# Kernel optimization log

Hardware: AMD Instinct MI355X
Metric: run time of the kernel (lower is better)

Reference implementation:

```python
import jax, jax.numpy as jnp
import numpy as np

B, N, DX, E, H, HD, KH, FF = 8, 8192, 2, 128, 8, 16, 32, 128
G1, G2, PMAX = 32, 32, 32


def _ln(x, g, b):
    mu = jnp.mean(x, axis=-1, keepdims=True)
    var = jnp.mean((x - mu) ** 2, axis=-1, keepdims=True)
    return (x - mu) * jax.lax.rsqrt(var + 1e-5) * g + b


def _cumcount_row(idx):
    # for each element, number of earlier elements with the same value (stable)
    n = idx.shape[0]
    order = jnp.argsort(idx)  # stable
    si = idx[order]
    ar = jnp.arange(n)
    is_start = jnp.concatenate([jnp.ones((1,), bool), si[1:] != si[:-1]])
    seg_start = jax.lax.associative_scan(jnp.maximum, jnp.where(is_start, ar, 0))
    return jnp.zeros(n, jnp.int32).at[order].set((ar - seg_start).astype(jnp.int32))


def _forward(x, z, latent, Wq, Wk, Wv, Wo, bo, kW1, kb1, kW2, kb2,
             lnq_g, lnq_b, lnk_g, lnk_b, ln2_g, ln2_b, fW1, fb1, fW2, fb2,
             grid_n1, grid_n2, max_patch, num_heads):
    Bb, Nn, dx = x.shape
    e = latent.shape[0]
    dims = (grid_n1, grid_n2)
    M = grid_n1 * grid_n2
    P = max_patch
    h = num_heads
    hd = Wq.shape[1] // h
    # grid range from data (margin = 0), regular grid via linspace
    mins = [jnp.min(x[:, :, i]) for i in range(dx)]
    maxs = [jnp.max(x[:, :, i]) for i in range(dx)]
    axes = [jnp.linspace(mins[i], maxs[i], dims[i]) for i in range(dx)]
    x_grid = jnp.stack(jnp.meshgrid(*axes, indexing="ij"), axis=-1)  # [G1,G2,dx]
    x_grid_flat = x_grid.reshape(M, dx)
    # nearest grid cell per point: regular grid -> per-dim rounding
    flat = None
    for i in range(dx):
        step = (maxs[i] - mins[i]) / (dims[i] - 1)
        ii = jnp.clip(jnp.round((x[..., i] - mins[i]) / step), 0, dims[i] - 1).astype(jnp.int32)
        flat = ii if flat is None else flat * dims[i] + ii
    cell = flat  # [B,N]
    cumc = jax.vmap(_cumcount_row)(cell)          # slot within cell
    slot = jnp.where(cumc < P, cumc, P)           # overflow -> dummy slot (dropped)
    bidx = jnp.broadcast_to(jnp.arange(Bb)[:, None], (Bb, Nn))
    # scatter points into per-cell padded neighbour sets [B, M, P, d]
    jx = jnp.zeros((Bb, M, P + 1, dx), x.dtype).at[bidx, cell, slot].set(x)[:, :, :P]
    jz = jnp.zeros((Bb, M, P + 1, e), z.dtype).at[bidx, cell, slot].set(z)[:, :, :P]
    msk = jnp.zeros((Bb, M, P + 1), bool).at[bidx, cell, slot].set(True)[:, :, :P]
    xg = jnp.broadcast_to(x_grid_flat[None], (Bb, M, dx))
    zg = jnp.broadcast_to(latent[None, None, :], (Bb, M, e))
    # concatenate_x_grid=True: grid token prepended, always attended
    joint_x = jnp.concatenate([xg[:, :, None, :], jx], axis=2).reshape(Bb * M, P + 1, dx)
    joint_z = jnp.concatenate([zg[:, :, None, :], jz], axis=2).reshape(Bb * M, P + 1, e)
    att_mask = jnp.concatenate([jnp.ones((Bb, M, 1), bool), msk], axis=2).reshape(Bb * M, P + 1)
    xq = xg.reshape(Bb * M, 1, dx)
    zq = zg.reshape(Bb * M, 1, e)
    T = Bb * M
    # masked translation-equivariant cross-attention (pre-norm layer)
    q = jnp.einsum("tqe,ef->tqf", _ln(zq, lnq_g, lnq_b), Wq).reshape(T, 1, h, hd)
    zk_n = _ln(joint_z, lnk_g, lnk_b)
    k = jnp.einsum("tke,ef->tkf", zk_n, Wk).reshape(T, P + 1, h, hd)
    v = jnp.einsum("tke,ef->tkf", zk_n, Wv).reshape(T, P + 1, h, hd)
    dots = jnp.einsum("tqhd,tkhd->thqk", q, k) / jnp.sqrt(jnp.asarray(hd, q.dtype))
    diff = joint_x[:, None, :, :] - xq[:, :, None, :]            # [T,1,P+1,dx]
    kb = jnp.maximum(diff @ kW1 + kb1, 0.0) @ kW2 + kb2          # kernel bias [T,1,P+1,h]
    dots = dots + jnp.transpose(kb, (0, 3, 1, 2))
    dots = jnp.where(att_mask[:, None, None, :], dots, -1e9)
    A = jax.nn.softmax(dots, axis=-1)                            # [T,h,1,P+1]
    out = jnp.einsum("thqk,tkhd->tqhd", A, v).reshape(T, 1, h * hd)
    z_new = zq + out @ Wo + bo
    z_new = z_new + (jnp.maximum(_ln(z_new, ln2_g, ln2_b) @ fW1 + fb1, 0.0) @ fW2 + fb2)
    x_new = jnp.einsum("tqk,tkd->tqd", jnp.mean(A, axis=1), joint_x)  # TE location update
    x_grid_out = x_new.reshape(Bb, grid_n1, grid_n2, dx)
    z_grid_out = z_new.reshape(Bb, grid_n1, grid_n2, e)
    return (x_grid_out, z_grid_out)


def setup_inputs():
    key = jax.random.key(0)
    ks = jax.random.split(key, 12)
    s = 0.05
    return {
        "x": jax.random.uniform(ks[0], (B, N, DX), jnp.float32),
        "z": jax.random.normal(ks[1], (B, N, E), jnp.float32),
        "grid_n1": G1, "grid_n2": G2, "max_patch": PMAX, "num_heads": H,
        "latent": jax.random.normal(ks[2], (E,), jnp.float32),
        "Wq": jax.random.normal(ks[3], (E, H * HD), jnp.float32) * s,
        "Wk": jax.random.normal(ks[4], (E, H * HD), jnp.float32) * s,
        "Wv": jax.random.normal(ks[5], (E, H * HD), jnp.float32) * s,
        "Wo": jax.random.normal(ks[6], (H * HD, E), jnp.float32) * s,
        "bo": jnp.zeros((E,), jnp.float32),
        "kW1": jax.random.normal(ks[7], (DX, KH), jnp.float32) * s,
        "kb1": jnp.zeros((KH,), jnp.float32),
        "kW2": jax.random.normal(ks[8], (KH, H), jnp.float32) * s,
        "kb2": jnp.zeros((H,), jnp.float32),
        "lnq_g": jnp.ones((E,), jnp.float32), "lnq_b": jnp.zeros((E,), jnp.float32),
        "lnk_g": jnp.ones((E,), jnp.float32), "lnk_b": jnp.zeros((E,), jnp.float32),
        "ln2_g": jnp.ones((E,), jnp.float32), "ln2_b": jnp.zeros((E,), jnp.float32),
        "fW1": jax.random.normal(ks[9], (E, FF), jnp.float32) * s,
        "fb1": jnp.zeros((FF,), jnp.float32),
        "fW2": jax.random.normal(ks[10], (FF, E), jnp.float32) * s,
        "fb2": jnp.zeros((E,), jnp.float32),
    }


def reference(x, z, grid_n1, grid_n2, max_patch, num_heads, latent, Wq, Wk, Wv, Wo, bo,
              kW1, kb1, kW2, kb2, lnq_g, lnq_b, lnk_g, lnk_b, ln2_g, ln2_b,
              fW1, fb1, fW2, fb2):
    return _forward(x, z, latent, Wq, Wk, Wv, Wo, bo, kW1, kb1, kW2, kb2,
                    lnq_g, lnq_b, lnk_g, lnk_b, ln2_g, ln2_b, fW1, fb1, fW2, fb2,
                    grid_n1, grid_n2, max_patch, num_heads)
```

## Files before the change

### kernel.cpp

```cpp
#include <hip/hip_runtime.h>
#include <stdint.h>

#define NB 8
#define NN 8192
#define NE 128
#define NH 8
#define NHD 16
#define NKH 32
#define NFF 128
#define NG 32
#define NM 1024
#define NP 32
#define NT 8192
#define NPTS 65536

typedef __attribute__((ext_vector_type(8))) short bf16x8_t;
typedef __attribute__((ext_vector_type(4))) float f32x4_t;

#define WS_MM      0
#define WS_D0      64
#define WS_Q       128
#define WS_VG      640
#define WS_PART    1152
#define WS_CNT     2048
#define WS_CELL    34816
#define WS_PIDX    296960
#define WS_WVT     1345536
#define WS_WOT     1411072
#define WS_FW1T    1443840
#define WS_FW2T    1476608
#define WS_WKQT    1509376
#define WS_SCORES  1513472
#define WS_KV      4194304

__device__ __forceinline__ unsigned short f2bf(float f) {
    unsigned u = __float_as_uint(f);
    u += 0x7FFFu + ((u >> 16) & 1u);
    return (unsigned short)(u >> 16);
}
__device__ __forceinline__ float bflo(unsigned w) { return __uint_as_float(w << 16); }
__device__ __forceinline__ float bfhi(unsigned w) { return __uint_as_float(w & 0xFFFF0000u); }

__global__ __launch_bounds__(256) void k_setup(
        const float* __restrict__ x,
        const float* __restrict__ Wk, const float* __restrict__ Wv, const float* __restrict__ Wo,
        const float* __restrict__ fW1, const float* __restrict__ fW2,
        const float* __restrict__ latent, const float* __restrict__ Wq,
        const float* __restrict__ lnq_g, const float* __restrict__ lnq_b,
        const float* __restrict__ lnk_g, const float* __restrict__ lnk_b,
        const float* __restrict__ kb1, const float* __restrict__ kW2, const float* __restrict__ kb2,
        int* __restrict__ cnt,
        unsigned short* __restrict__ WvT, unsigned short* __restrict__ WoT,
        unsigned short* __restrict__ fW1T, unsigned short* __restrict__ fW2T,
        float* __restrict__ ws_q, float* __restrict__ ws_vg, float* __restrict__ ws_d0,
        unsigned short* __restrict__ WkqT,
        float4* __restrict__ part) {
    int blk = blockIdx.x;
    int t = threadIdx.x;
    if (blk < 16) {
        __shared__ float s_t[64][65];
        const float* src; unsigned short* dst;
        int n0, k0;
        if (blk < 4) {
            int tn = blk >> 1, tk = blk & 1;
            n0 = tn * 64; k0 = tk * 64;
            src = Wv; dst = WvT;
        } else {
            int m = (blk - 4) >> 2, s4 = (blk - 4) & 3;
            int tn = s4 >> 1, tk = s4 & 1;
            n0 = tn * 64; k0 = tk * 64;
            src = (m == 0) ? Wo : (m == 1) ? fW1 : fW2;
            dst = (m == 0) ? WoT : (m == 1) ? fW1T : fW2T;
        }
        int tx = t & 63, ty = t >> 6;
        #pragma unroll
        for (int r = 0; r < 16; ++r) {
            int kr = r * 4 + ty;
            s_t[kr][tx] = src[(k0 + kr) * 128 + n0 + tx];
        }
        __syncthreads();
        #pragma unroll
        for (int r = 0; r < 16; ++r) {
            int nr = r * 4 + ty;
            dst[(n0 + nr) * 128 + k0 + tx] = f2bf(s_t[tx][nr]);
        }
    } else if (blk < 48) {
        int idx = (blk - 16) * 256 + t;
        cnt[idx] = 0;
    } else if (blk == 48) {
        __shared__ float s_qn[128], s_kn[128], s_q[128], s_kg[128];
        __shared__ float s_mu, s_rstd;
        if (t < 64) {
            float v0 = latent[t], v1 = latent[t + 64];
            float s = v0 + v1;
            for (int m = 32; m > 0; m >>= 1) s += __shfl_xor(s, m);
            float mu = s * (1.0f / 128.0f);
            float d0 = v0 - mu, d1 = v1 - mu;
            float q = d0 * d0 + d1 * d1;
            for (int m = 32; m > 0; m >>= 1) q += __shfl_xor(q, m);
            if (t == 0) { s_mu = mu; s_rstd = rsqrtf(q * (1.0f / 128.0f) + 1e-5f); }
        }
        __syncthreads();
        if (t < 128) {
            float nv = (latent[t] - s_mu) * s_rstd;
            s_qn[t] = nv * lnq_g[t] + lnq_b[t];
            s_kn[t] = nv * lnk_g[t] + lnk_b[t];
        }
        __syncthreads();
        if (t < 128) {
            float aq = 0.f, ak = 0.f, av = 0.f;
            for (int e = 0; e < 128; ++e) {
                aq += s_qn[e] * Wq[e * 128 + t];
                ak += s_kn[e] * Wk[e * 128 + t];
                av += s_kn[e] * Wv[e * 128 + t];
            }
            s_q[t] = aq; s_kg[t] = ak;
            ws_q[t] = aq; ws_vg[t] = av;
        }
        __syncthreads();
        if (t < 128) {
            const float* wr = Wk + t * 128;
            #pragma unroll
            for (int h = 0; h < 8; ++h) {
                float a = 0.f;
                #pragma unroll
                for (int d = 0; d < 16; ++d) a += wr[h * 16 + d] * s_q[h * 16 + d];
                WkqT[h * 128 + t] = f2bf(a * 0.25f);
                WkqT[(h + 8) * 128 + t] = 0;
            }
        }
        if (t < 8) {
            float acc = 0.f;
            for (int d = 0; d < 16; ++d) acc += s_q[t * 16 + d] * s_kg[t * 16 + d];
            float kb0 = kb2[t];
            for (int j = 0; j < 32; ++j) kb0 += fmaxf(kb1[j], 0.f) * kW2[j * 8 + t];
            ws_d0[t] = acc * 0.25f + kb0;
        }
    } else {
        __shared__ float s_red[4][4];
        int pb = blk - 49;
        const float4* xp = (const float4*)x + pb * 1024;
        float mn0 = 1e30f, mx0 = -1e30f, mn1 = 1e30f, mx1 = -1e30f;
        #pragma unroll
        for (int it = 0; it < 4; ++it) {
            float4 v = xp[it * 256 + t];
            mn0 = fminf(mn0, fminf(v.x, v.z)); mx0 = fmaxf(mx0, fmaxf(v.x, v.z));
            mn1 = fminf(mn1, fminf(v.y, v.w)); mx1 = fmaxf(mx1, fmaxf(v.y, v.w));
        }
        #pragma unroll
        for (int m = 32; m > 0; m >>= 1) {
            mn0 = fminf(mn0, __shfl_xor(mn0, m)); mx0 = fmaxf(mx0, __shfl_xor(mx0, m));
            mn1 = fminf(mn1, __shfl_xor(mn1, m)); mx1 = fmaxf(mx1, __shfl_xor(mx1, m));
        }
        int w = t >> 6;
        if ((t & 63) == 0) {
            s_red[w][0] = mn0; s_red[w][1] = mn1; s_red[w][2] = mx0; s_red[w][3] = mx1;
        }
        __syncthreads();
        if (t == 0) {
            float a0 = fminf(fminf(s_red[0][0], s_red[1][0]), fminf(s_red[2][0], s_red[3][0]));
            float a1 = fminf(fminf(s_red[0][1], s_red[1][1]), fminf(s_red[2][1], s_red[3][1]));
            float b0 = fmaxf(fmaxf(s_red[0][2], s_red[1][2]), fmaxf(s_red[2][2], s_red[3][2]));
            float b1 = fmaxf(fmaxf(s_red[0][3], s_red[1][3]), fmaxf(s_red[2][3], s_red[3][3]));
            part[pb] = make_float4(a0, a1, b0, b1);
        }
    }
}

__global__ __launch_bounds__(256) void k_binkv(
        const float* __restrict__ x, const float* __restrict__ z,
        const float4* __restrict__ part, float* __restrict__ mm,
        const float* __restrict__ lnk_g, const float* __restrict__ lnk_b,
        const unsigned short* __restrict__ WkqT,
        const float* __restrict__ kW1, const float* __restrict__ kb1,
        const float* __restrict__ kW2, const float* __restrict__ kb2,
        const unsigned short* __restrict__ WvT, unsigned short* __restrict__ kv,
        float* __restrict__ scores,
        int* __restrict__ cell, int* __restrict__ cnt, int* __restrict__ ptIdx) {
    int t = threadIdx.x;
    if (blockIdx.x >= 1024) {
        int l = t & 63;
        float mn0 = 1e30f, mn1 = 1e30f, mx0 = -1e30f, mx1 = -1e30f;
        if (l < 32) { float4 p = part[l]; mn0 = p.x; mn1 = p.y; mx0 = p.z; mx1 = p.w; }
        #pragma unroll
        for (int m = 32; m > 0; m >>= 1) {
            mn0 = fminf(mn0, __shfl_xor(mn0, m)); mx0 = fmaxf(mx0, __shfl_xor(mx0, m));
            mn1 = fminf(mn1, __shfl_xor(mn1, m)); mx1 = fmaxf(mx1, __shfl_xor(mx1, m));
        }
        if (blockIdx.x == 1024 && t == 0) {
            mm[0] = mn0; mm[1] = mn1; mm[2] = mx0; mm[3] = mx1;
        }
        int i = (blockIdx.x - 1024) * 256 + t;
        float st0 = (mx0 - mn0) / 31.0f, st1 = (mx1 - mn1) / 31.0f;
        float2 xv = ((const float2*)x)[i];
        int i0 = (int)rintf((xv.x - mn0) / st0); i0 = min(max(i0, 0), 31);
        int i1 = (int)rintf((xv.y - mn1) / st1); i1 = min(max(i1, 0), 31);
        int c = i0 * 32 + i1;
        cell[i] = c;
        int bb = i >> 13;
        int slot = atomicAdd(&cnt[bb * NM + c], 1);
        if (slot < NP) ptIdx[(bb * NM + c) * NP + slot] = i & (NN - 1);
        return;
    }
    __shared__ unsigned short s_zn[64][136];
    __shared__ unsigned short s_stage[4][16][68];
    int w = t >> 6, lane = t & 63;
    long base = (long)blockIdx.x * 64;
    int sub = lane >> 5;
    int lq = lane & 31;
    int mrow = lane & 15, quad = lane >> 4;

    float mn0 = 1e30f, mn1 = 1e30f, mx0 = -1e30f, mx1 = -1e30f;
    if (lane < 32) { float4 p = part[lane]; mn0 = p.x; mn1 = p.y; mx0 = p.z; mx1 = p.w; }
    #pragma unroll
    for (int m = 32; m > 0; m >>= 1) {
        mn0 = fminf(mn0, __shfl_xor(mn0, m)); mx0 = fmaxf(mx0, __shfl_xor(mx0, m));
        mn1 = fminf(mn1, __shfl_xor(mn1, m)); mx1 = fmaxf(mx1, __shfl_xor(mx1, m));
    }
    int ptl = w * 16 + mrow;
    float2 xv2 = ((const float2*)x)[base + ptl];

    int th = w >> 1, fh = w & 1;
    bf16x8_t afrag[4][4];
    #pragma unroll
    for (int j = 0; j < 4; ++j) {
        const unsigned short* ap = WvT + ((fh * 4 + j) * 16 + mrow) * 128 + quad * 8;
        #pragma unroll
        for (int kc = 0; kc < 4; ++kc)
            afrag[j][kc] = *(const bf16x8_t*)(ap + kc * 32);
    }
    bf16x8_t sfrag[4];
    #pragma unroll
    for (int kc = 0; kc < 4; ++kc)
        sfrag[kc] = *(const bf16x8_t*)(WkqT + mrow * 128 + kc * 32 + quad * 8);

    float4 g4 = ((const float4*)lnk_g)[lq];
    float4 b4 = ((const float4*)lnk_b)[lq];
    float4 v[8];
    #pragma unroll
    for (int i = 0; i < 8; ++i) {
        int pl = w * 16 + i * 2 + sub;
        v[i] = ((const float4*)z)[(base + pl) * 32 + lq];
    }
    #pragma unroll
    for (int i = 0; i < 8; ++i) {
        int pl = w * 16 + i * 2 + sub;
        float sum = v[i].x + v[i].y + v[i].z + v[i].w;
        float ssq = v[i].x * v[i].x + v[i].y * v[i].y + v[i].z * v[i].z + v[i].w * v[i].w;
        #pragma unroll
        for (int m = 1; m < 32; m <<= 1) {
            sum += __shfl_xor(sum, m);
            ssq += __shfl_xor(ssq, m);
        }
        float mu = sum * (1.0f / 128.0f);
        float var = fmaxf(ssq * (1.0f / 128.0f) - mu * mu, 0.0f);
        float rstd = rsqrtf(var + 1e-5f);
        float n0 = (v[i].x - mu) * rstd * g4.x + b4.x;
        float n1 = (v[i].y - mu) * rstd * g4.y + b4.y;
        float n2 = (v[i].z - mu) * rstd * g4.z + b4.z;
        float n3 = (v[i].w - mu) * rstd * g4.w + b4.w;
        unsigned d0 = (unsigned)f2bf(n0) | ((unsigned)f2bf(n1) << 16);
        unsigned d1 = (unsigned)f2bf(n2) | ((unsigned)f2bf(n3) << 16);
        *(uint2*)&s_zn[pl][lq * 4] = make_uint2(d0, d1);
    }
    __syncthreads();

    #pragma unroll
    for (int tau = 0; tau < 2; ++tau) {
        int trow = th * 32 + tau * 16;
        bf16x8_t bfrag[4];
        #pragma unroll
        for (int kc = 0; kc < 4; ++kc)
            bfrag[kc] = *(const bf16x8_t*)&s_zn[trow + mrow][kc * 32 + quad * 8];
        #pragma unroll
        for (int j = 0; j < 4; ++j) {
            f32x4_t acc = {0.f, 0.f, 0.f, 0.f};
            #pragma unroll
            for (int kc = 0; kc < 4; ++kc)
                acc = __builtin_amdgcn_mfma_f32_16x16x32_bf16(afrag[j][kc], bfrag[kc], acc, 0, 0, 0);
            unsigned d0 = (unsigned)f2bf(acc[0]) | ((unsigned)f2bf(acc[1]) << 16);
            unsigned d1 = (unsigned)f2bf(acc[2]) | ((unsigned)f2bf(acc[3]) << 16);
            *(uint2*)&s_stage[w][mrow][j * 16 + quad * 4] = make_uint2(d0, d1);
        }
        int tok = lane >> 3, u = lane & 7;
        long tk0 = base + trow;
        uint4 ra = *(const uint4*)&s_stage[w][tok][u * 8];
        *(uint4*)(kv + (tk0 + tok) * 128 + fh * 64 + u * 8) = ra;
        uint4 rb = *(const uint4*)&s_stage[w][tok + 8][u * 8];
        *(uint4*)(kv + (tk0 + tok + 8) * 128 + fh * 64 + u * 8) = rb;
    }

    f32x4_t sacc = {0.f, 0.f, 0.f, 0.f};
    {
        bf16x8_t sb[4];
        #pragma unroll
        for (int kc = 0; kc < 4; ++kc)
            sb[kc] = *(const bf16x8_t*)&s_zn[w * 16 + mrow][kc * 32 + quad * 8];
        #pragma unroll
        for (int kc = 0; kc < 4; ++kc)
            sacc = __builtin_amdgcn_mfma_f32_16x16x32_bf16(sfrag[kc], sb[kc], sacc, 0, 0, 0);
    }

    {
        float st0 = (mx0 - mn0) / 31.0f, st1 = (mx1 - mn1) / 31.0f;
        int i0 = (int)rintf((xv2.x - mn0) / st0); i0 = min(max(i0, 0), 31);
        int i1 = (int)rintf((xv2.y - mn1) / st1); i1 = min(max(i1, 0), 31);
        float cx0 = (i0 == 31) ? mx0 : mn0 + i0 * st0;
        float cx1 = (i1 == 31) ? mx1 : mn1 + i1 * st1;
        float d0 = xv2.x - cx0, d1 = xv2.y - cx1;
        float k0 = 0.f, k1 = 0.f, k2 = 0.f, k3 = 0.f, k4 = 0.f, k5 = 0.f, k6 = 0.f, k7 = 0.f;
        #pragma unroll
        for (int jj = 0; jj < 8; ++jj) {
            int j = quad * 8 + jj;
            float hj = fmaf(d0, kW1[j], fmaf(d1, kW1[32 + j], kb1[j]));
            hj = fmaxf(hj, 0.f);
            float4 w2a = *(const float4*)(kW2 + j * 8);
            float4 w2b = *(const float4*)(kW2 + j * 8 + 4);
            k0 = fmaf(hj, w2a.x, k0); k1 = fmaf(hj, w2a.y, k1);
            k2 = fmaf(hj, w2a.z, k2); k3 = fmaf(hj, w2a.w, k3);
            k4 = fmaf(hj, w2b.x, k4); k5 = fmaf(hj, w2b.y, k5);
            k6 = fmaf(hj, w2b.z, k6); k7 = fmaf(hj, w2b.w, k7);
        }
        k0 += __shfl_xor(k0, 16); k0 += __shfl_xor(k0, 32);
        k1 += __shfl_xor(k1, 16); k1 += __shfl_xor(k1, 32);
        k2 += __shfl_xor(k2, 16); k2 += __shfl_xor(k2, 32);
        k3 += __shfl_xor(k3, 16); k3 += __shfl_xor(k3, 32);
        k4 += __shfl_xor(k4, 16); k4 += __shfl_xor(k4, 32);
        k5 += __shfl_xor(k5, 16); k5 += __shfl_xor(k5, 32);
        k6 += __shfl_xor(k6, 16); k6 += __shfl_xor(k6, 32);
        k7 += __shfl_xor(k7, 16); k7 += __shfl_xor(k7, 32);
        if (quad == 0) {
            float4 kb2v = ((const float4*)kb2)[0];
            float4 o;
            o.x = sacc[0] + k0 + kb2v.x; o.y = sacc[1] + k1 + kb2v.y;
            o.z = sacc[2] + k2 + kb2v.z; o.w = sacc[3] + k3 + kb2v.w;
            *(float4*)(scores + ((size_t)(base + ptl)) * 8) = o;
        } else if (quad == 1) {
            float4 kb2v = ((const float4*)kb2)[1];
            float4 o;
            o.x = sacc[0] + k4 + kb2v.x; o.y = sacc[1] + k5 + kb2v.y;
            o.z = sacc[2] + k6 + kb2v.z; o.w = sacc[3] + k7 + kb2v.w;
            *(float4*)(scores + ((size_t)(base + ptl)) * 8 + 4) = o;
        }
    }
}

__global__ __launch_bounds__(256) void k_attn(const float* __restrict__ x,
        const int* __restrict__ cell, const int* __restrict__ cnt, int* __restrict__ ptIdx,
        const float* __restrict__ mm, const unsigned short* __restrict__ kv,
        const float* __restrict__ scores,
        const float* __restrict__ ws_vg, const float* __restrict__ ws_d0,
        const float* __restrict__ latent, const float* __restrict__ bo,
        const float* __restrict__ ln2_g, const float* __restrict__ ln2_b,
        const float* __restrict__ fb1, const float* __restrict__ fb2,
        const unsigned short* __restrict__ WoT, const unsigned short* __restrict__ fW1T,
        const unsigned short* __restrict__ fW2T,
        float* __restrict__ xout, float* __restrict__ zout) {
    __shared__ unsigned short s_a[16][136];
    __shared__ unsigned short s_a2[16][136];
    __shared__ float s_z[4][128];
    __shared__ float s_lat[128], s_g2[128], s_b2[128], s_fb1v[128], s_fb2v[128];
    int t = threadIdx.x;
    int l = t & 63;
    int w = t >> 6;
    if (t < 128) {
        s_lat[t] = latent[t] + bo[t];
        s_g2[t] = ln2_g[t]; s_b2[t] = ln2_b[t];
        s_fb1v[t] = fb1[t]; s_fb2v[t] = fb2[t];
    }
    int bm = blockIdx.x * 4 + w;
    int b = bm >> 10;
    int h = l >> 3, jp = l & 7;

    float mn0 = mm[0], mn1 = mm[1], mx0 = mm[2], mx1 = mm[3];
    int i0 = (bm & 1023) >> 5, i1 = bm & 31;
    float st0 = (mx0 - mn0) / 31.0f, st1 = (mx1 - mn1) / 31.0f;
    float xg0 = (i0 == 31) ? mx0 : mn0 + i0 * st0;
    float xg1 = (i1 == 31) ? mx1 : mn1 + i1 * st1;
    int craw = cnt[bm];
    int c = min(craw, NP);
    if (craw > NP) {
        int mycell = bm & 1023;
        const int* cb = cell + b * NN;
        int run = 0;
        for (int ch = 0; ch < NN / 64 && run < NP; ++ch) {
            int n = ch * 64 + l;
            bool match = (cb[n] == mycell);
            unsigned long long mask = __ballot(match);
            if (match) {
                int rank = run + __popcll(mask & ((1ull << l) - 1ull));
                if (rank < NP) ptIdx[bm * NP + rank] = n;
            }
            run += __popcll(mask);
        }
    }

    float vg0 = ws_vg[2 * l], vg1 = ws_vg[2 * l + 1];
    float ag = ws_d0[h];

    int idxreg = 0; float x0r = 0.f, x1r = 0.f;
    if (l < c) {
        idxreg = ptIdx[bm * NP + l];
        float2 xv = ((const float2*)x)[(size_t)b * NN + idxreg];
        x0r = xv.x; x1r = xv.y;
    }

    float areg[4];
    areg[0] = areg[1] = areg[2] = areg[3] = -1e30f;
    #pragma unroll
    for (int g = 0; g < 4; ++g) {
        if (c > g * 8) {
            int key = g * 8 + jp;
            int idxk = __shfl(idxreg, key);
            if (key < c)
                areg[g] = scores[((size_t)b * NN + idxk) * 8 + h];
        }
    }
    unsigned vreg[16];
    #pragma unroll
    for (int g = 0; g < 2; ++g) {
        if (c > g * 8) {
            #pragma unroll
            for (int k8 = 0; k8 < 8; ++k8) {
                int key = g * 8 + k8;
                if (key < c) {
                    int idxk = __shfl(idxreg, key);
                    vreg[key] = ((const unsigned*)kv)[((size_t)(b * NN + idxk) << 6) + l];
                }
            }
        }
    }

    float mx = fmaxf(fmaxf(areg[0], areg[1]), fmaxf(areg[2], areg[3]));
    mx = fmaxf(mx, ag);
    mx = fmaxf(mx, __shfl_xor(mx, 1));
    mx = fmaxf(mx, __shfl_xor(mx, 2));
    mx = fmaxf(mx, __shfl_xor(mx, 4));
    float e0 = __expf(areg[0] - mx), e1 = __expf(areg[1] - mx);
    float e2 = __expf(areg[2] - mx), e3 = __expf(areg[3] - mx);
    float eg = __expf(ag - mx);
    float s = e0 + e1 + e2 + e3;
    s += __shfl_xor(s, 1);
    s += __shfl_xor(s, 2);
    s += __shfl_xor(s, 4);
    s += eg;
    float inv = 1.0f / s;

    float accA = eg * inv * vg0, accB = eg * inv * vg1;
    #pragma unroll
    for (int g = 0; g < 2; ++g) {
        if (c > g * 8) {
            float em = (g == 0) ? e0 : e1;
            #pragma unroll
            for (int k8 = 0; k8 < 8; ++k8) {
                int key = g * 8 + k8;
                if (key < c) {
                    float a = __shfl(em, (l & 56) | k8) * inv;
                    unsigned vw = vreg[key];
                    accA = fmaf(a, bflo(vw), accA);
                    accB = fmaf(a, bfhi(vw), accB);
                }
            }
        }
    }
    #pragma unroll
    for (int g = 2; g < 4; ++g) {
        if (c > g * 8) {
            float em = (g == 2) ? e2 : e3;
            #pragma unroll
            for (int k8 = 0; k8 < 8; ++k8) {
                int key = g * 8 + k8;
                if (key < c) {
                    int idxk = __shfl(idxreg, key);
                    const unsigned* rowp = (const unsigned*)kv + ((size_t)(b * NN + idxk) << 6);
                    unsigned vw = rowp[l];
                    float a = __shfl(em, (l & 56) | k8) * inv;
                    accA = fmaf(a, bflo(vw), accA);
                    accB = fmaf(a, bfhi(vw), accB);
                }
            }
        }
    }
    unsigned ow = ((unsigned)f2bf(accB) << 16) | (unsigned)f2bf(accA);
    *(unsigned*)&s_a[w][2 * l] = ow;

    float s0 = e0 * inv, s1 = e1 * inv, s2 = e2 * inv, s3 = e3 * inv, sg = eg * inv;
    #pragma unroll
    for (int m = 8; m <= 32; m <<= 1) {
        s0 += __shfl_xor(s0, m); s1 += __shfl_xor(s1, m);
        s2 += __shfl_xor(s2, m); s3 += __shfl_xor(s3, m);
        sg += __shfl_xor(sg, m);
    }
    float px0 = 0.f, px1 = 0.f;
    {
        float xx0, xx1;
        xx0 = __shfl(x0r, jp);      xx1 = __shfl(x1r, jp);
        px0 = fmaf(s0, xx0, px0);   px1 = fmaf(s0, xx1, px1);
        xx0 = __shfl(x0r, jp + 8);  xx1 = __shfl(x1r, jp + 8);
        px0 = fmaf(s1, xx0, px0);   px1 = fmaf(s1, xx1, px1);
        xx0 = __shfl(x0r, jp + 16); xx1 = __shfl(x1r, jp + 16);
        px0 = fmaf(s2, xx0, px0);   px1 = fmaf(s2, xx1, px1);
        xx0 = __shfl(x0r, jp + 24); xx1 = __shfl(x1r, jp + 24);
        px0 = fmaf(s3, xx0, px0);   px1 = fmaf(s3, xx1, px1);
    }
    px0 += __shfl_xor(px0, 1); px1 += __shfl_xor(px1, 1);
    px0 += __shfl_xor(px0, 2); px1 += __shfl_xor(px1, 2);
    px0 += __shfl_xor(px0, 4); px1 += __shfl_xor(px1, 4);
    if (l == 0) {
        xout[bm * 2]     = (px0 + sg * xg0) * 0.125f;
        xout[bm * 2 + 1] = (px1 + sg * xg1) * 0.125f;
    }

    __syncthreads();
    int mrow = l & 15, quad = l >> 4;
    int base4 = blockIdx.x * 4;
    {
        bf16x8_t a[4];
        #pragma unroll
        for (int kc = 0; kc < 4; ++kc)
            a[kc] = *(const bf16x8_t*)&s_a[mrow][kc * 32 + quad * 8];
        #pragma unroll
        for (int cc = 0; cc < 2; ++cc) {
            int ct = w * 2 + cc;
            f32x4_t acc = {0.f, 0.f, 0.f, 0.f};
            const unsigned short* bp = WoT + (ct * 16 + mrow) * 128 + quad * 8;
            #pragma unroll
            for (int kc = 0; kc < 4; ++kc)
                acc = __builtin_amdgcn_mfma_f32_16x16x32_bf16(a[kc], *(const bf16x8_t*)(bp + kc * 32), acc, 0, 0, 0);
            if (quad == 0) {
                int f = ct * 16 + mrow;
                #pragma unroll
                for (int r = 0; r < 4; ++r) s_z[r][f] = acc[r] + s_lat[f];
            }
        }
    }
    __syncthreads();
    {
        float v0 = s_z[w][l], v1 = s_z[w][l + 64];
        float ssum = v0 + v1;
        #pragma unroll
        for (int m = 32; m > 0; m >>= 1) ssum += __shfl_xor(ssum, m);
        float mu = ssum * (1.0f / 128.0f);
        float d0 = v0 - mu, d1 = v1 - mu;
        float qq = d0 * d0 + d1 * d1;
        #pragma unroll
        for (int m = 32; m > 0; m >>= 1) qq += __shfl_xor(qq, m);
        float rstd = rsqrtf(qq * (1.0f / 128.0f) + 1e-5f);
        s_a2[w][l]      = f2bf(d0 * rstd * s_g2[l] + s_b2[l]);
        s_a2[w][l + 64] = f2bf(d1 * rstd * s_g2[l + 64] + s_b2[l + 64]);
    }
    __syncthreads();
    {
        bf16x8_t a[4];
        #pragma unroll
        for (int kc = 0; kc < 4; ++kc)
            a[kc] = *(const bf16x8_t*)&s_a2[mrow][kc * 32 + quad * 8];
        #pragma unroll
        for (int cc = 0; cc < 2; ++cc) {
            int ct = w * 2 + cc;
            f32x4_t acc = {0.f, 0.f, 0.f, 0.f};
            const unsigned short* bp = fW1T + (ct * 16 + mrow) * 128 + quad * 8;
            #pragma unroll
            for (int kc = 0; kc < 4; ++kc)
                acc = __builtin_amdgcn_mfma_f32_16x16x32_bf16(a[kc], *(const bf16x8_t*)(bp + kc * 32), acc, 0, 0, 0);
            if (quad == 0) {
                int f = ct * 16 + mrow;
                #pragma unroll
                for (int r = 0; r < 4; ++r)
                    s_a[r][f] = f2bf(fmaxf(acc[r] + s_fb1v[f], 0.f));
            }
        }
    }
    __syncthreads();
    {
        bf16x8_t a[4];
        #pragma unroll
        for (int kc = 0; kc < 4; ++kc)
            a[kc] = *(const bf16x8_t*)&s_a[mrow][kc * 32 + quad * 8];
        #pragma unroll
        for (int cc = 0; cc < 2; ++cc) {
            int ct = w * 2 + cc;
            f32x4_t acc = {0.f, 0.f, 0.f, 0.f};
            const unsigned short* bp = fW2T + (ct * 16 + mrow) * 128 + quad * 8;
            #pragma unroll
            for (int kc = 0; kc < 4; ++kc)
                acc = __builtin_amdgcn_mfma_f32_16x16x32_bf16(a[kc], *(const bf16x8_t*)(bp + kc * 32), acc, 0, 0, 0);
            if (quad == 0) {
                int f = ct * 16 + mrow;
                #pragma unroll
                for (int r = 0; r < 4; ++r)
                    zout[(base4 + r) * 128 + f] = s_z[r][f] + acc[r] + s_fb2v[f];
            }
        }
    }
}

extern "C" void kernel_launch(void* const* d_in, const int* in_sizes, int n_in,
                              void* d_out, int out_size, void* d_ws, size_t ws_size,
                              hipStream_t stream) {
    const float* x     = (const float*)d_in[0];
    const float* z     = (const float*)d_in[1];
    const float* latent= (const float*)d_in[6];
    const float* Wq    = (const float*)d_in[7];
    const float* Wk    = (const float*)d_in[8];
    const float* Wv    = (const float*)d_in[9];
    const float* Wo    = (const float*)d_in[10];
    const float* bo    = (const float*)d_in[11];
    const float* kW1   = (const float*)d_in[12];
    const float* kb1   = (const float*)d_in[13];
    const float* kW2   = (const float*)d_in[14];
    const float* kb2   = (const float*)d_in[15];
    const float* lnq_g = (const float*)d_in[16];
    const float* lnq_b = (const float*)d_in[17];
    const float* lnk_g = (const float*)d_in[18];
    const float* lnk_b = (const float*)d_in[19];
    const float* ln2_g = (const float*)d_in[20];
    const float* ln2_b = (const float*)d_in[21];
    const float* fW1   = (const float*)d_in[22];
    const float* fb1   = (const float*)d_in[23];
    const float* fW2   = (const float*)d_in[24];
    const float* fb2   = (const float*)d_in[25];

    uint8_t* ws = (uint8_t*)d_ws;
    float* mm     = (float*)(ws + WS_MM);
    float* ws_d0  = (float*)(ws + WS_D0);
    float* ws_q   = (float*)(ws + WS_Q);
    float* ws_vg  = (float*)(ws + WS_VG);
    float4* part  = (float4*)(ws + WS_PART);
    int* cnt      = (int*)(ws + WS_CNT);
    int* cell     = (int*)(ws + WS_CELL);
    int* ptIdx    = (int*)(ws + WS_PIDX);
    unsigned short* WvT  = (unsigned short*)(ws + WS_WVT);
    unsigned short* WoT  = (unsigned short*)(ws + WS_WOT);
    unsigned short* fW1T = (unsigned short*)(ws + WS_FW1T);
    unsigned short* fW2T = (unsigned short*)(ws + WS_FW2T);
    unsigned short* WkqT = (unsigned short*)(ws + WS_WKQT);
    float* scores = (float*)(ws + WS_SCORES);
    unsigned short* kv   = (unsigned short*)(ws + WS_KV);

    float* xout = (float*)d_out;
    float* zout = (float*)d_out + 16384;

    k_setup <<<81,   256, 0, stream>>>(x, Wk, Wv, Wo, fW1, fW2, latent, Wq,
                                       lnq_g, lnq_b, lnk_g, lnk_b, kb1, kW2, kb2,
                                       cnt, WvT, WoT, fW1T, fW2T, ws_q, ws_vg, ws_d0,
                                       WkqT, part);
    k_binkv <<<1280, 256, 0, stream>>>(x, z, part, mm, lnk_g, lnk_b, WkqT,
                                       kW1, kb1, kW2, kb2, WvT, kv, scores,
                                       cell, cnt, ptIdx);
    k_attn  <<<2048, 256, 0, stream>>>(x, cell, cnt, ptIdx, mm, kv, scores,
                                       ws_vg, ws_d0,
                                       latent, bo, ln2_g, ln2_b, fb1, fb2,
                                       WoT, fW1T, fW2T, xout, zout);
}
```

Before: 178.6 us.

## Process 16 cells per block in k_attn to fill MFMA rows

Each wave now loops over four grid cells, so a block handles 16 cells instead of 4 and launches with a quarter of the blocks. The MFMA output projection, LayerNorm and FFN stages then use all 16 rows of the 16x16 tiles rather than wasting 12 of them. Weight loads are amortized over four times as many cells. The cost is fewer blocks, so less parallelism to hide the latency of the gather loop, and the serialized per-wave attention loop gets longer.

```diff
diff --git a/kernel.cpp b/kernel.cpp
--- a/kernel.cpp
+++ b/kernel.cpp
@@ -358,162 +358,166 @@
         float* __restrict__ xout, float* __restrict__ zout) {
     __shared__ unsigned short s_a[16][136];
     __shared__ unsigned short s_a2[16][136];
-    __shared__ float s_z[4][128];
+    __shared__ float s_z[16][128];
     __shared__ float s_lat[128], s_g2[128], s_b2[128], s_fb1v[128], s_fb2v[128];
     int t = threadIdx.x;
     int l = t & 63;
     int w = t >> 6;
+    int h = l >> 3, jp = l & 7;
+    int base16 = blockIdx.x * 16;
+
     if (t < 128) {
         s_lat[t] = latent[t] + bo[t];
         s_g2[t] = ln2_g[t]; s_b2[t] = ln2_b[t];
         s_fb1v[t] = fb1[t]; s_fb2v[t] = fb2[t];
     }
-    int bm = blockIdx.x * 4 + w;
-    int b = bm >> 10;
-    int h = l >> 3, jp = l & 7;
 
     float mn0 = mm[0], mn1 = mm[1], mx0 = mm[2], mx1 = mm[3];
-    int i0 = (bm & 1023) >> 5, i1 = bm & 31;
     float st0 = (mx0 - mn0) / 31.0f, st1 = (mx1 - mn1) / 31.0f;
-    float xg0 = (i0 == 31) ? mx0 : mn0 + i0 * st0;
-    float xg1 = (i1 == 31) ? mx1 : mn1 + i1 * st1;
-    int craw = cnt[bm];
-    int c = min(craw, NP);
-    if (craw > NP) {
-        int mycell = bm & 1023;
-        const int* cb = cell + b * NN;
-        int run = 0;
-        for (int ch = 0; ch < NN / 64 && run < NP; ++ch) {
-            int n = ch * 64 + l;
-            bool match = (cb[n] == mycell);
-            unsigned long long mask = __ballot(match);
-            if (match) {
-                int rank = run + __popcll(mask & ((1ull << l) - 1ull));
-                if (rank < NP) ptIdx[bm * NP + rank] = n;
-            }
-            run += __popcll(mask);
-        }
-    }
-
     float vg0 = ws_vg[2 * l], vg1 = ws_vg[2 * l + 1];
     float ag = ws_d0[h];
 
-    int idxreg = 0; float x0r = 0.f, x1r = 0.f;
-    if (l < c) {
-        idxreg = ptIdx[bm * NP + l];
-        float2 xv = ((const float2*)x)[(size_t)b * NN + idxreg];
-        x0r = xv.x; x1r = xv.y;
-    }
-
-    float areg[4];
-    areg[0] = areg[1] = areg[2] = areg[3] = -1e30f;
     #pragma unroll
-    for (int g = 0; g < 4; ++g) {
-        if (c > g * 8) {
-            int key = g * 8 + jp;
-            int idxk = __shfl(idxreg, key);
-            if (key < c)
-                areg[g] = scores[((size_t)b * NN + idxk) * 8 + h];
-        }
-    }
-    unsigned vreg[16];
-    #pragma unroll
-    for (int g = 0; g < 2; ++g) {
-        if (c > g * 8) {
-            #pragma unroll
-            for (int k8 = 0; k8 < 8; ++k8) {
-                int key = g * 8 + k8;
-                if (key < c) {
-                    int idxk = __shfl(idxreg, key);
-                    vreg[key] = ((const unsigned*)kv)[((size_t)(b * NN + idxk) << 6) + l];
+    for (int it = 0; it < 4; ++it) {
+        int bm = base16 + w * 4 + it;
+        int b = bm >> 10;
+        int i0 = (bm & 1023) >> 5, i1 = bm & 31;
+        float xg0 = (i0 == 31) ? mx0 : mn0 + i0 * st0;
+        float xg1 = (i1 == 31) ? mx1 : mn1 + i1 * st1;
+        int craw = cnt[bm];
+        int c = min(craw, NP);
+        if (craw > NP) {
+            int mycell = bm & 1023;
+            const int* cb = cell + b * NN;
+            int run = 0;
+            for (int ch = 0; ch < NN / 64 && run < NP; ++ch) {
+                int n = ch * 64 + l;
+                bool match = (cb[n] == mycell);
+                unsigned long long mask = __ballot(match);
+                if (match) {
+                    int rank = run + __popcll(mask & ((1ull << l) - 1ull));
+                    if (rank < NP) ptIdx[bm * NP + rank] = n;
                 }
-            }
-        }
-    }
-
-    float mx = fmaxf(fmaxf(areg[0], areg[1]), fmaxf(areg[2], areg[3]));
-    mx = fmaxf(mx, ag);
-    mx = fmaxf(mx, __shfl_xor(mx, 1));
-    mx = fmaxf(mx, __shfl_xor(mx, 2));
-    mx = fmaxf(mx, __shfl_xor(mx, 4));
-    float e0 = __expf(areg[0] - mx), e1 = __expf(areg[1] - mx);
-    float e2 = __expf(areg[2] - mx), e3 = __expf(areg[3] - mx);
-    float eg = __expf(ag - mx);
-    float s = e0 + e1 + e2 + e3;
-    s += __shfl_xor(s, 1);
-    s += __shfl_xor(s, 2);
-    s += __shfl_xor(s, 4);
-    s += eg;
-    float inv = 1.0f / s;
-
-    float accA = eg * inv * vg0, accB = eg * inv * vg1;
-    #pragma unroll
-    for (int g = 0; g < 2; ++g) {
-        if (c > g * 8) {
-            float em = (g == 0) ? e0 : e1;
-            #pragma unroll
-            for (int k8 = 0; k8 < 8; ++k8) {
-                int key = g * 8 + k8;
-                if (key < c) {
-                    float a = __shfl(em, (l & 56) | k8) * inv;
-                    unsigned vw = vreg[key];
-                    accA = fmaf(a, bflo(vw), accA);
-                    accB = fmaf(a, bfhi(vw), accB);
+                run += __popcll(mask);
+            }
+        }
+
+        int idxreg = 0; float x0r = 0.f, x1r = 0.f;
+        if (l < c) {
+            idxreg = ptIdx[bm * NP + l];
+            float2 xv = ((const float2*)x)[(size_t)b * NN + idxreg];
+            x0r = xv.x; x1r = xv.y;
+        }
+
+        float areg[4];
+        areg[0] = areg[1] = areg[2] = areg[3] = -1e30f;
+        #pragma unroll
+        for (int g = 0; g < 4; ++g) {
+            if (c > g * 8) {
+                int key = g * 8 + jp;
+                int idxk = __shfl(idxreg, key);
+                if (key < c)
+                    areg[g] = scores[((size_t)b * NN + idxk) * 8 + h];
+            }
+        }
+        unsigned vreg[16];
+        #pragma unroll
+        for (int g = 0; g < 2; ++g) {
+            if (c > g * 8) {
+                #pragma unroll
+                for (int k8 = 0; k8 < 8; ++k8) {
+                    int key = g * 8 + k8;
+                    if (key < c) {
+                        int idxk = __shfl(idxreg, key);
+                        vreg[key] = ((const unsigned*)kv)[((size_t)(b * NN + idxk) << 6) + l];
+                    }
                 }
             }
         }
-    }
-    #pragma unroll
-    for (int g = 2; g < 4; ++g) {
-        if (c > g * 8) {
-            float em = (g == 2) ? e2 : e3;
-            #pragma unroll
-            for (int k8 = 0; k8 < 8; ++k8) {
-                int key = g * 8 + k8;
-                if (key < c) {
-                    int idxk = __shfl(idxreg, key);
-                    const unsigned* rowp = (const unsigned*)kv + ((size_t)(b * NN + idxk) << 6);
-                    unsigned vw = rowp[l];
-                    float a = __shfl(em, (l & 56) | k8) * inv;
-                    accA = fmaf(a, bflo(vw), accA);
-                    accB = fmaf(a, bfhi(vw), accB);
+
+        float mx = fmaxf(fmaxf(areg[0], areg[1]), fmaxf(areg[2], areg[3]));
+        mx = fmaxf(mx, ag);
+        mx = fmaxf(mx, __shfl_xor(mx, 1));
+        mx = fmaxf(mx, __shfl_xor(mx, 2));
+        mx = fmaxf(mx, __shfl_xor(mx, 4));
+        float e0 = __expf(areg[0] - mx), e1 = __expf(areg[1] - mx);
+        float e2 = __expf(areg[2] - mx), e3 = __expf(areg[3] - mx);
+        float eg = __expf(ag - mx);
+        float s = e0 + e1 + e2 + e3;
+        s += __shfl_xor(s, 1);
+        s += __shfl_xor(s, 2);
+        s += __shfl_xor(s, 4);
+        s += eg;
+        float inv = 1.0f / s;
+
+        float accA = eg * inv * vg0, accB = eg * inv * vg1;
+        #pragma unroll
+        for (int g = 0; g < 2; ++g) {
+            if (c > g * 8) {
+                float em = (g == 0) ? e0 : e1;
+                #pragma unroll
+                for (int k8 = 0; k8 < 8; ++k8) {
+                    int key = g * 8 + k8;
+                    if (key < c) {
+                        float a = __shfl(em, (l & 56) | k8) * inv;
+                        unsigned vw = vreg[key];
+                        accA = fmaf(a, bflo(vw), accA);
+                        accB = fmaf(a, bfhi(vw), accB);
+                    }
                 }
             }
         }
-    }
-    unsigned ow = ((unsigned)f2bf(accB) << 16) | (unsigned)f2bf(accA);
-    *(unsigned*)&s_a[w][2 * l] = ow;
-
-    float s0 = e0 * inv, s1 = e1 * inv, s2 = e2 * inv, s3 = e3 * inv, sg = eg * inv;
-    #pragma unroll
-    for (int m = 8; m <= 32; m <<= 1) {
-        s0 += __shfl_xor(s0, m); s1 += __shfl_xor(s1, m);
-        s2 += __shfl_xor(s2, m); s3 += __shfl_xor(s3, m);
-        sg += __shfl_xor(sg, m);
-    }
-    float px0 = 0.f, px1 = 0.f;
-    {
-        float xx0, xx1;
-        xx0 = __shfl(x0r, jp);      xx1 = __shfl(x1r, jp);
-        px0 = fmaf(s0, xx0, px0);   px1 = fmaf(s0, xx1, px1);
-        xx0 = __shfl(x0r, jp + 8);  xx1 = __shfl(x1r, jp + 8);
-        px0 = fmaf(s1, xx0, px0);   px1 = fmaf(s1, xx1, px1);
-        xx0 = __shfl(x0r, jp + 16); xx1 = __shfl(x1r, jp + 16);
-        px0 = fmaf(s2, xx0, px0);   px1 = fmaf(s2, xx1, px1);
-        xx0 = __shfl(x0r, jp + 24); xx1 = __shfl(x1r, jp + 24);
-        px0 = fmaf(s3, xx0, px0);   px1 = fmaf(s3, xx1, px1);
-    }
-    px0 += __shfl_xor(px0, 1); px1 += __shfl_xor(px1, 1);
-    px0 += __shfl_xor(px0, 2); px1 += __shfl_xor(px1, 2);
-    px0 += __shfl_xor(px0, 4); px1 += __shfl_xor(px1, 4);
-    if (l == 0) {
-        xout[bm * 2]     = (px0 + sg * xg0) * 0.125f;
-        xout[bm * 2 + 1] = (px1 + sg * xg1) * 0.125f;
+        #pragma unroll
+        for (int g = 2; g < 4; ++g) {
+            if (c > g * 8) {
+                float em = (g == 2) ? e2 : e3;
+                #pragma unroll
+                for (int k8 = 0; k8 < 8; ++k8) {
+                    int key = g * 8 + k8;
+                    if (key < c) {
+                        int idxk = __shfl(idxreg, key);
+                        const unsigned* rowp = (const unsigned*)kv + ((size_t)(b * NN + idxk) << 6);
+                        unsigned vw = rowp[l];
+                        float a = __shfl(em, (l & 56) | k8) * inv;
+                        accA = fmaf(a, bflo(vw), accA);
+                        accB = fmaf(a, bfhi(vw), accB);
+                    }
+                }
+            }
+        }
+        unsigned ow = ((unsigned)f2bf(accB) << 16) | (unsigned)f2bf(accA);
+        *(unsigned*)&s_a[w * 4 + it][2 * l] = ow;
+
+        float s0 = e0 * inv, s1 = e1 * inv, s2 = e2 * inv, s3 = e3 * inv, sg = eg * inv;
+        #pragma unroll
+        for (int m = 8; m <= 32; m <<= 1) {
+            s0 += __shfl_xor(s0, m); s1 += __shfl_xor(s1, m);
+            s2 += __shfl_xor(s2, m); s3 += __shfl_xor(s3, m);
+            sg += __shfl_xor(sg, m);
+        }
+        float px0 = 0.f, px1 = 0.f;
+        {
+            float xx0, xx1;
+            xx0 = __shfl(x0r, jp);      xx1 = __shfl(x1r, jp);
+            px0 = fmaf(s0, xx0, px0);   px1 = fmaf(s0, xx1, px1);
+            xx0 = __shfl(x0r, jp + 8);  xx1 = __shfl(x1r, jp + 8);
+            px0 = fmaf(s1, xx0, px0);   px1 = fmaf(s1, xx1, px1);
+            xx0 = __shfl(x0r, jp + 16); xx1 = __shfl(x1r, jp + 16);
+            px0 = fmaf(s2, xx0, px0);   px1 = fmaf(s2, xx1, px1);
+            xx0 = __shfl(x0r, jp + 24); xx1 = __shfl(x1r, jp + 24);
+            px0 = fmaf(s3, xx0, px0);   px1 = fmaf(s3, xx1, px1);
+        }
+        px0 += __shfl_xor(px0, 1); px1 += __shfl_xor(px1, 1);
+        px0 += __shfl_xor(px0, 2); px1 += __shfl_xor(px1, 2);
+        px0 += __shfl_xor(px0, 4); px1 += __shfl_xor(px1, 4);
+        if (l == 0) {
+            xout[bm * 2]     = (px0 + sg * xg0) * 0.125f;
+            xout[bm * 2 + 1] = (px1 + sg * xg1) * 0.125f;
+        }
     }
 
     __syncthreads();
     int mrow = l & 15, quad = l >> 4;
-    int base4 = blockIdx.x * 4;
     {
         bf16x8_t a[4];
         #pragma unroll
@@ -527,27 +531,32 @@
             #pragma unroll
             for (int kc = 0; kc < 4; ++kc)
                 acc = __builtin_amdgcn_mfma_f32_16x16x32_bf16(a[kc], *(const bf16x8_t*)(bp + kc * 32), acc, 0, 0, 0);
-            if (quad == 0) {
-                int f = ct * 16 + mrow;
-                #pragma unroll
-                for (int r = 0; r < 4; ++r) s_z[r][f] = acc[r] + s_lat[f];
+            int f = ct * 16 + mrow;
+            #pragma unroll
+            for (int r = 0; r < 4; ++r) {
+                int row = quad * 4 + r;
+                s_z[row][f] = acc[r] + s_lat[f];
             }
         }
     }
     __syncthreads();
     {
-        float v0 = s_z[w][l], v1 = s_z[w][l + 64];
-        float ssum = v0 + v1;
-        #pragma unroll
-        for (int m = 32; m > 0; m >>= 1) ssum += __shfl_xor(ssum, m);
-        float mu = ssum * (1.0f / 128.0f);
-        float d0 = v0 - mu, d1 = v1 - mu;
-        float qq = d0 * d0 + d1 * d1;
-        #pragma unroll
-        for (int m = 32; m > 0; m >>= 1) qq += __shfl_xor(qq, m);
-        float rstd = rsqrtf(qq * (1.0f / 128.0f) + 1e-5f);
-        s_a2[w][l]      = f2bf(d0 * rstd * s_g2[l] + s_b2[l]);
-        s_a2[w][l + 64] = f2bf(d1 * rstd * s_g2[l + 64] + s_b2[l + 64]);
+        #pragma unroll
+        for (int i = 0; i < 4; ++i) {
+            int row = w * 4 + i;
+            float v0 = s_z[row][l], v1 = s_z[row][l + 64];
+            float ssum = v0 + v1;
+            #pragma unroll
+            for (int m = 32; m > 0; m >>= 1) ssum += __shfl_xor(ssum, m);
+            float mu = ssum * (1.0f / 128.0f);
+            float d0 = v0 - mu, d1 = v1 - mu;
+            float qq = d0 * d0 + d1 * d1;
+            #pragma unroll
+            for (int m = 32; m > 0; m >>= 1) qq += __shfl_xor(qq, m);
+            float rstd = rsqrtf(qq * (1.0f / 128.0f) + 1e-5f);
+            s_a2[row][l]      = f2bf(d0 * rstd * s_g2[l] + s_b2[l]);
+            s_a2[row][l + 64] = f2bf(d1 * rstd * s_g2[l + 64] + s_b2[l + 64]);
+        }
     }
     __syncthreads();
     {
@@ -563,11 +572,11 @@
             #pragma unroll
             for (int kc = 0; kc < 4; ++kc)
                 acc = __builtin_amdgcn_mfma_f32_16x16x32_bf16(a[kc], *(const bf16x8_t*)(bp + kc * 32), acc, 0, 0, 0);
-            if (quad == 0) {
-                int f = ct * 16 + mrow;
-                #pragma unroll
-                for (int r = 0; r < 4; ++r)
-                    s_a[r][f] = f2bf(fmaxf(acc[r] + s_fb1v[f], 0.f));
+            int f = ct * 16 + mrow;
+            #pragma unroll
+            for (int r = 0; r < 4; ++r) {
+                int row = quad * 4 + r;
+                s_a[row][f] = f2bf(fmaxf(acc[r] + s_fb1v[f], 0.f));
             }
         }
     }
@@ -585,11 +594,11 @@
             #pragma unroll
             for (int kc = 0; kc < 4; ++kc)
                 acc = __builtin_amdgcn_mfma_f32_16x16x32_bf16(a[kc], *(const bf16x8_t*)(bp + kc * 32), acc, 0, 0, 0);
-            if (quad == 0) {
-                int f = ct * 16 + mrow;
-                #pragma unroll
-                for (int r = 0; r < 4; ++r)
-                    zout[(base4 + r) * 128 + f] = s_z[r][f] + acc[r] + s_fb2v[f];
+            int f = ct * 16 + mrow;
+            #pragma unroll
+            for (int r = 0; r < 4; ++r) {
+                int row = quad * 4 + r;
+                zout[(size_t)(base16 + row) * 128 + f] = s_z[row][f] + acc[r] + s_fb2v[f];
             }
         }
     }
@@ -648,7 +657,7 @@
     k_binkv <<<1280, 256, 0, stream>>>(x, z, part, mm, lnk_g, lnk_b, WkqT,
                                        kW1, kb1, kW2, kb2, WvT, kv, scores,
                                        cell, cnt, ptIdx);
-    k_attn  <<<2048, 256, 0, stream>>>(x, cell, cnt, ptIdx, mm, kv, scores,
+    k_attn  <<<512,  256, 0, stream>>>(x, cell, cnt, ptIdx, mm, kv, scores,
                                        ws_vg, ws_d0,
                                        latent, bo, ln2_g, ln2_b, fb1, fb2,
                                        WoT, fW1T, fW2T, xout, zout);
```

Measured after the change: 170.9 us (median of 2 runs). -4.3%, faster.
